# Optimization experiments

Measured on AMD Instinct MI355X. Metric: run time of the kernel, lower is better.

The kernel has to match this reference:

```python
import jax, jax.numpy as jnp
import numpy as np

BITS = 8
KQA_TOPK_PROP = 0.25
NUM_HEADS = 16


def quantize_pc(t, n_bits=BITS):
    # per-channel fake quantization over the last dim (torch quantize with
    # quantization_type='per_channel')
    q_max = 2 ** (n_bits - 1) - 1
    scales = jnp.max(jnp.abs(t), axis=-1, keepdims=True)
    scales = jnp.maximum(scales, 1e-5) / q_max
    return jnp.clip(jnp.round(t / scales), -q_max - 1, q_max) * scales


def setup_inputs() -> dict:
    key = jax.random.key(0)
    ks = jax.random.split(key, 5)
    B, N, C = 4, 1024, 1024
    x = jax.random.normal(ks[0], (B, N, C), dtype=jnp.float32)
    W_qkv = jax.random.normal(ks[1], (3 * C, C), dtype=jnp.float32) * (C ** -0.5)
    b_qkv = jax.random.normal(ks[2], (3 * C,), dtype=jnp.float32) * 0.02
    W_proj = jax.random.normal(ks[3], (C, C), dtype=jnp.float32) * (C ** -0.5)
    b_proj = jax.random.normal(ks[4], (C,), dtype=jnp.float32) * 0.02
    return {"x": x, "W_qkv": W_qkv, "b_qkv": b_qkv, "W_proj": W_proj, "b_proj": b_proj}


def _split_qkv(lin, B, N, H, hd):
    # [B,N,3C] -> (3,B,H,N,hd)
    t = jnp.transpose(lin.reshape(B, N, 3, H, hd), (2, 0, 3, 1, 4))
    return t[0], t[1], t[2]


def reference(x, W_qkv, b_qkv, W_proj, b_proj):
    B, N, C = x.shape
    H = NUM_HEADS
    hd = C // H
    scale = hd ** -0.5

    # --- quantized QKV path (KeyQueryAttention) ---
    q_x = quantize_pc(x)
    q_w = quantize_pc(W_qkv)
    q_b = quantize_pc(b_qkv)
    q_lin = quantize_pc(jnp.einsum('bnc,oc->bno', q_x, q_w) + q_b)
    q_q, q_k, _ = _split_qkv(q_lin, B, N, H, hd)
    q_attn = jnp.einsum('bhnd,bhmd->bhnm', q_q, q_k) * scale

    # --- topk-sliced partial-matmul approximation path ---
    r1 = int(C * KQA_TOPK_PROP) + 1  # channel slice of x / W_qkv
    topk_lin = jnp.einsum('bnc,oc->bno', x[:, :, :r1], W_qkv[:, :r1]) + b_qkv
    topk_q, topk_k, _ = _split_qkv(topk_lin, B, N, H, hd)
    r2 = int(hd * KQA_TOPK_PROP) + 1  # slices the SEQUENCE dim (dim 2), as in the torch code
    topk_attn = jnp.einsum('bhnd,bhmd->bhnm', topk_q[:, :, :r2], topk_k[:, :, :r2]) * scale

    # --- exact attention path (used for the output) ---
    lin = jnp.einsum('bnc,oc->bno', x, W_qkv) + b_qkv
    q, k, v = _split_qkv(lin, B, N, H, hd)
    attn = jax.nn.softmax(jnp.einsum('bhnd,bhmd->bhnm', q, k) * scale, axis=-1)
    out = jnp.einsum('bhnm,bhmd->bhnd', attn, v)  # [B,H,N,hd]
    out = jnp.transpose(out, (0, 2, 1, 3)).reshape(B, N, C)
    out = jnp.einsum('bnc,oc->bno', out, W_proj) + b_proj
    return out, q_attn, topk_attn
```

## Files before the change

### kernel.cpp

```cpp
#include <hip/hip_runtime.h>
#include <stdint.h>

typedef __bf16 bf16x8 __attribute__((ext_vector_type(8)));
typedef float f32x4 __attribute__((ext_vector_type(4)));
typedef int i32x4 __attribute__((ext_vector_type(4)));
typedef unsigned short u16;

#define DEVI static __device__ __forceinline__

DEVI u16 bfu(float f){
  unsigned u = __builtin_bit_cast(unsigned, f);
  unsigned r = u + 0x7fffu + ((u >> 16) & 1u);
  return (u16)(r >> 16);
}
DEVI unsigned packbf(float a, float b){
  return (unsigned)bfu(a) | ((unsigned)bfu(b) << 16);
}

DEVI void gload16(const void* g, void* s){
  __builtin_amdgcn_global_load_lds(
      (const __attribute__((address_space(1))) unsigned int*)g,
      (__attribute__((address_space(3))) unsigned int*)s, 16, 0, 0);
}

DEVI float blockReduceMax(float v, float* sred){
  for (int off = 32; off; off >>= 1) v = fmaxf(v, __shfl_xor(v, off));
  int w = threadIdx.x >> 6;
  if ((threadIdx.x & 63) == 0) sred[w] = v;
  __syncthreads();
  float r = fmaxf(fmaxf(sred[0], sred[1]), fmaxf(sred[2], sred[3]));
  __syncthreads();
  return r;
}

DEVI void quant_row_body(const float* __restrict__ in, int8_t* __restrict__ qo,
                         u16* __restrict__ bo, float* __restrict__ so, int row, float* sred){
  const int t = threadIdx.x;
  const float4 v = *(const float4*)(in + (size_t)row * 1024 + t * 4);
  float am = fmaxf(fmaxf(fabsf(v.x), fabsf(v.y)), fmaxf(fabsf(v.z), fabsf(v.w)));
  am = blockReduceMax(am, sred);
  const float s = fmaxf(am, 1e-5f) / 127.0f;
  if (t == 0) so[row] = s;
  char4 q;
  q.x = (int8_t)(int)fminf(fmaxf(rintf(v.x / s), -128.f), 127.f);
  q.y = (int8_t)(int)fminf(fmaxf(rintf(v.y / s), -128.f), 127.f);
  q.z = (int8_t)(int)fminf(fmaxf(rintf(v.z / s), -128.f), 127.f);
  q.w = (int8_t)(int)fminf(fmaxf(rintf(v.w / s), -128.f), 127.f);
  *(char4*)(qo + (size_t)row * 1024 + t * 4) = q;
  ushort4 h; h.x = bfu(v.x); h.y = bfu(v.y); h.z = bfu(v.z); h.w = bfu(v.w);
  *(ushort4*)(bo + (size_t)row * 1024 + t * 4) = h;
}

DEVI void quant_b_body(const float* __restrict__ b, float* __restrict__ qb, float* sred){
  const int t = threadIdx.x;
  float am = 0.f;
  for (int i = t; i < 3072; i += 256) am = fmaxf(am, fabsf(b[i]));
  am = blockReduceMax(am, sred);
  const float s = fmaxf(am, 1e-5f) / 127.0f;
  for (int i = t; i < 3072; i += 256){
    float q = fminf(fmaxf(rintf(b[i] / s), -128.f), 127.f);
    qb[i] = q * s;
  }
}

DEVI void topk_lin_body(int idx, const float* __restrict__ x, const float* __restrict__ Wq,
                        const float* __restrict__ bq, float* __restrict__ tlin){
  const int o = idx & 2047, bn = idx >> 11;
  const int b_ = bn / 17, n = bn % 17;
  const float* xr = x + ((size_t)b_ * 1024 + n) * 1024;
  const float* wr = Wq + (size_t)o * 1024;
  const float4* x4 = (const float4*)xr;
  const float4* w4 = (const float4*)wr;
  float s = 0.f;
  for (int c = 0; c < 64; c++){
    float4 a = x4[c], b = w4[c];
    s += a.x * b.x + a.y * b.y + a.z * b.z + a.w * b.w;
  }
  s += xr[256] * wr[256];
  tlin[idx] = s + bq[o];
}

DEVI void gemm_i8_body(char* smem, int bid, const int8_t* __restrict__ A, const int8_t* __restrict__ Bm,
    const float* __restrict__ sx, const float* __restrict__ sw, const float* __restrict__ qb,
    float* __restrict__ out){
  int8_t* As = (int8_t*)smem;
  int8_t* Bs = (int8_t*)(smem + 8192);
  const int t = threadIdx.x, l = t & 63, w = t >> 6;
  const int m0 = (bid / 24) * 128, n0 = (bid % 24) * 128;
  const int wm = (w >> 1) * 64, wn = (w & 1) * 64, lr = l & 15, lg = l >> 4;
  i32x4 acc[4][4];
  i32x4 z = {0, 0, 0, 0};
  for (int i = 0; i < 4; i++) for (int j = 0; j < 4; j++) acc[i][j] = z;
  for (int kt = 0; kt < 16; kt++){
    __syncthreads();
    for (int it = 0; it < 2; it++){
      int c = w * 2 + it;
      int idx = c * 64 + l;
      int r = idx >> 2, boff = (idx & 3) * 16;
      gload16(A  + (size_t)(m0 + r) * 1024 + kt * 64 + boff, &As[c * 1024]);
      gload16(Bm + (size_t)(n0 + r) * 1024 + kt * 64 + boff, &Bs[c * 1024]);
    }
    __syncthreads();
    i32x4 a[4], b[4];
    for (int i = 0; i < 4; i++) a[i] = *(const i32x4*)(&As[(wm + i * 16 + lr) * 64 + lg * 16]);
    for (int j = 0; j < 4; j++) b[j] = *(const i32x4*)(&Bs[(wn + j * 16 + lr) * 64 + lg * 16]);
    for (int i = 0; i < 4; i++)
      for (int j = 0; j < 4; j++)
        acc[i][j] = __builtin_amdgcn_mfma_i32_16x16x64_i8(a[i], b[j], acc[i][j], 0, 0, 0);
  }
  for (int i = 0; i < 4; i++){
    int row = m0 + wm + i * 16 + lg * 4;
    for (int j = 0; j < 4; j++){
      int col = n0 + wn + j * 16 + lr;
      float swc = sw[col], qbc = qb[col];
      for (int r = 0; r < 4; r++)
        out[(size_t)(row + r) * 3072 + col] = (float)acc[i][j][r] * sx[row + r] * swc + qbc;
    }
  }
}

template<int MODE>
DEVI void gemm_bf16_body(char* smem, int bid, const u16* __restrict__ A, const u16* __restrict__ Bm,
    const float* __restrict__ bias, void* __restrict__ outp, int K, int N, int nxb){
  u16* As = (u16*)smem;
  u16* Bs = (u16*)(smem + 8192);
  const int t = threadIdx.x, l = t & 63, w = t >> 6;
  const int m0 = (bid / nxb) * 128, n0 = (bid % nxb) * 128;
  const int wm = (w >> 1) * 64, wn = (w & 1) * 64, lr = l & 15, lg = l >> 4;
  f32x4 acc[4][4];
  f32x4 z = {0.f, 0.f, 0.f, 0.f};
  for (int i = 0; i < 4; i++) for (int j = 0; j < 4; j++) acc[i][j] = z;
  const int nkt = K >> 5;
  for (int kt = 0; kt < nkt; kt++){
    __syncthreads();
    for (int it = 0; it < 2; it++){
      int c = w * 2 + it;
      int idx = c * 64 + l;
      int r = idx >> 2, off = (idx & 3) * 8;
      gload16(A  + (size_t)(m0 + r) * K + kt * 32 + off, &As[c * 512]);
      gload16(Bm + (size_t)(n0 + r) * K + kt * 32 + off, &Bs[c * 512]);
    }
    __syncthreads();
    bf16x8 a[4], b[4];
    for (int i = 0; i < 4; i++) a[i] = *(const bf16x8*)(&As[(wm + i * 16 + lr) * 32 + lg * 8]);
    for (int j = 0; j < 4; j++) b[j] = *(const bf16x8*)(&Bs[(wn + j * 16 + lr) * 32 + lg * 8]);
    for (int i = 0; i < 4; i++)
      for (int j = 0; j < 4; j++)
        acc[i][j] = __builtin_amdgcn_mfma_f32_16x16x32_bf16(a[i], b[j], acc[i][j], 0, 0, 0);
  }
  for (int i = 0; i < 4; i++){
    int row = m0 + wm + i * 16 + lg * 4;
    for (int j = 0; j < 4; j++){
      int col = n0 + wn + j * 16 + lr;
      float bc = bias[col];
      for (int r = 0; r < 4; r++){
        float v = acc[i][j][r] + bc;
        if (MODE == 0){
          int s = col >> 10, h = (col >> 6) & 15, d = col & 63;
          int b_ = (row + r) >> 10, n = (row + r) & 1023;
          ((u16*)outp)[(((size_t)(s * 64 + b_ * 16 + h)) * 1024 + n) * 64 + d] = bfu(v);
        } else {
          ((float*)outp)[(size_t)(row + r) * N + col] = v;
        }
      }
    }
  }
}

DEVI void topk_attn_body(int b2, const float* __restrict__ tlin, float* __restrict__ outp){
  const int idx = b2 * 256 + threadIdx.x;
  if (idx >= 4 * 16 * 17 * 17) return;
  const int mm = idx % 17; int rest = idx / 17;
  const int nn = rest % 17; rest /= 17;
  const int h = rest % 16; const int b_ = rest / 16;
  const float* tq = tlin + ((size_t)(b_ * 17 + nn)) * 2048 + h * 64;
  const float* tk = tlin + ((size_t)(b_ * 17 + mm)) * 2048 + 1024 + h * 64;
  float s = 0.f;
  for (int d = 0; d < 64; d++) s += tq[d] * tk[d];
  outp[71303168 + idx] = s * 0.125f;
}

DEVI void qlin_quant_body(float* sred, int row, const float* __restrict__ qlin,
                          float* __restrict__ s_ql, int8_t* __restrict__ iq, int8_t* __restrict__ ik){
  const int t = threadIdx.x;
  const float* rp = qlin + (size_t)row * 3072;
  float am = 0.f;
  for (int i = 0; i < 3; i++){
    float4 v = *(const float4*)(rp + t * 4 + i * 1024);
    am = fmaxf(am, fmaxf(fmaxf(fabsf(v.x), fabsf(v.y)), fmaxf(fabsf(v.z), fabsf(v.w))));
  }
  am = blockReduceMax(am, sred);
  const float s = fmaxf(am, 1e-5f) / 127.0f;
  if (t == 0) s_ql[row] = s;
  const int b_ = row >> 10, n = row & 1023;
  const int o0 = t * 8;
  int8_t* dst = (o0 < 1024) ? iq : ik;
  const int oo = o0 & 1023, h = oo >> 6, d = oo & 63;
  const size_t base = (((size_t)(b_ * 16 + h) * 1024 + n) * 64 + d);
  union { int8_t c[8]; unsigned long long u; } pk;
  for (int j = 0; j < 8; j++)
    pk.c[j] = (int8_t)(int)fminf(fmaxf(rintf(rp[o0 + j] / s), -128.f), 127.f);
  *(unsigned long long*)(dst + base) = pk.u;
}

DEVI void attn_body(u16* vt, int qt, int bz, const u16* __restrict__ qkv, u16* __restrict__ aout){
  const int t = threadIdx.x, l = t & 63, w = t >> 6, lr = l & 15, lg = l >> 4;
  const int b_ = bz >> 4, h = bz & 15;
  const u16* Q  = qkv + (size_t)bz * 65536;
  const u16* Kg = qkv + (size_t)(64 + bz) * 65536;
  const u16* Vg = qkv + (size_t)(128 + bz) * 65536;
  const int q0 = qt * 64 + w * 16;
  const bf16x8 bq0 = *(const bf16x8*)(Q + (size_t)(q0 + lr) * 64 + lg * 8);
  const bf16x8 bq1 = *(const bf16x8*)(Q + (size_t)(q0 + lr) * 64 + 32 + lg * 8);
  float m = -1e30f, lsum = 0.f;
  f32x4 o[4];
  f32x4 zf = {0.f, 0.f, 0.f, 0.f};
  for (int dt = 0; dt < 4; dt++) o[dt] = zf;
  const int hi = lg & 1, tt = lg >> 1;
  const int srcA = lr + 32 * hi, srcB = srcA + 16;
  const int vr = t >> 3, voff = (t & 7) * 8;
  {
    uint4 vv = *(const uint4*)(Vg + (size_t)vr * 64 + voff);
    const u16* pv = (const u16*)&vv;
    for (int j = 0; j < 8; j++) vt[(0 * 64 + voff + j) * 40 + vr] = pv[j];
  }
  __syncthreads();
  int cur = 0;
  for (int kv0 = 0; kv0 < 1024; kv0 += 32){
    const bf16x8 ak00 = *(const bf16x8*)(Kg + (size_t)(kv0 + lr) * 64 + lg * 8);
    const bf16x8 ak01 = *(const bf16x8*)(Kg + (size_t)(kv0 + lr) * 64 + 32 + lg * 8);
    const bf16x8 ak10 = *(const bf16x8*)(Kg + (size_t)(kv0 + 16 + lr) * 64 + lg * 8);
    const bf16x8 ak11 = *(const bf16x8*)(Kg + (size_t)(kv0 + 16 + lr) * 64 + 32 + lg * 8);
    const bool more = (kv0 + 32) < 1024;
    uint4 vn = {0, 0, 0, 0};
    if (more) vn = *(const uint4*)(Vg + (size_t)(kv0 + 32 + vr) * 64 + voff);
    f32x4 st[2];
    {
      f32x4 c = zf;
      c = __builtin_amdgcn_mfma_f32_16x16x32_bf16(ak00, bq0, c, 0, 0, 0);
      c = __builtin_amdgcn_mfma_f32_16x16x32_bf16(ak01, bq1, c, 0, 0, 0);
      st[0] = c;
      c = zf;
      c = __builtin_amdgcn_mfma_f32_16x16x32_bf16(ak10, bq0, c, 0, 0, 0);
      c = __builtin_amdgcn_mfma_f32_16x16x32_bf16(ak11, bq1, c, 0, 0, 0);
      st[1] = c;
    }
    float tmax = -1e30f;
    for (int kvt = 0; kvt < 2; kvt++)
      for (int r = 0; r < 4; r++){ st[kvt][r] *= 0.125f; tmax = fmaxf(tmax, st[kvt][r]); }
    tmax = fmaxf(tmax, __shfl_xor(tmax, 16));
    tmax = fmaxf(tmax, __shfl_xor(tmax, 32));
    const float mn = fmaxf(m, tmax);
    const float f = __expf(m - mn);
    m = mn;
    float p[2][4], psum = 0.f;
    for (int kvt = 0; kvt < 2; kvt++)
      for (int r = 0; r < 4; r++){ float e = __expf(st[kvt][r] - mn); p[kvt][r] = e; psum += e; }
    psum += __shfl_xor(psum, 16);
    psum += __shfl_xor(psum, 32);
    lsum = lsum * f + psum;
    for (int dt = 0; dt < 4; dt++) for (int r = 0; r < 4; r++) o[dt][r] *= f;
    int pk00 = (int)packbf(p[0][0], p[0][1]), pk01 = (int)packbf(p[0][2], p[0][3]);
    int pk10 = (int)packbf(p[1][0], p[1][1]), pk11 = (int)packbf(p[1][2], p[1][3]);
    int a0 = __shfl(pk00, srcA), a1 = __shfl(pk10, srcA);
    int b0 = __shfl(pk01, srcA), b1 = __shfl(pk11, srcA);
    int c0 = __shfl(pk00, srcB), c1 = __shfl(pk10, srcB);
    int d0 = __shfl(pk01, srcB), d1 = __shfl(pk11, srcB);
    union { unsigned u[4]; bf16x8 v; } bp;
    bp.u[0] = (unsigned)(tt ? a1 : a0);
    bp.u[1] = (unsigned)(tt ? b1 : b0);
    bp.u[2] = (unsigned)(tt ? c1 : c0);
    bp.u[3] = (unsigned)(tt ? d1 : d0);
    for (int dt = 0; dt < 4; dt++){
      bf16x8 av = *(const bf16x8*)(&vt[(cur * 64 + dt * 16 + lr) * 40 + lg * 8]);
      o[dt] = __builtin_amdgcn_mfma_f32_16x16x32_bf16(av, bp.v, o[dt], 0, 0, 0);
    }
    if (more){
      const u16* pv = (const u16*)&vn;
      for (int j = 0; j < 8; j++) vt[((cur ^ 1) * 64 + voff + j) * 40 + vr] = pv[j];
    }
    __syncthreads();
    cur ^= 1;
  }
  const float rn = 1.0f / lsum;
  for (int dt = 0; dt < 4; dt++){
    ushort4 hv;
    hv.x = bfu(o[dt][0] * rn); hv.y = bfu(o[dt][1] * rn);
    hv.z = bfu(o[dt][2] * rn); hv.w = bfu(o[dt][3] * rn);
    *(ushort4*)(aout + ((size_t)(b_ * 1024 + q0 + lr)) * 1024 + h * 64 + dt * 16 + lg * 4) = hv;
  }
}

DEVI void qattn_body(int b2, const int8_t* __restrict__ iq, const int8_t* __restrict__ ik,
    const float* __restrict__ s_ql, float* __restrict__ outp){
  const int t = threadIdx.x, l = t & 63, w = t >> 6, lr = l & 15, lg = l >> 4;
  const int n0 = (b2 & 7) * 128, m0 = ((b2 >> 3) & 7) * 128, bz = b2 >> 6;
  const int wm = (w >> 1) * 64, wn = (w & 1) * 64;
  const int b_ = bz >> 4;
  const int8_t* Aq = iq + (size_t)bz * 65536;
  const int8_t* Bk = ik + (size_t)bz * 65536;
  i32x4 a[4], b[4];
  for (int i = 0; i < 4; i++) a[i] = *(const i32x4*)(Aq + (size_t)(m0 + wm + i * 16 + lr) * 64 + lg * 16);
  for (int j = 0; j < 4; j++) b[j] = *(const i32x4*)(Bk + (size_t)(n0 + wn + j * 16 + lr) * 64 + lg * 16);
  float* op = outp + 4194304 + (size_t)bz * 1048576;
  i32x4 z = {0, 0, 0, 0};
  for (int i = 0; i < 4; i++){
    int row = m0 + wm + i * 16 + lg * 4;
    for (int j = 0; j < 4; j++){
      i32x4 acc = __builtin_amdgcn_mfma_i32_16x16x64_i8(a[i], b[j], z, 0, 0, 0);
      int col = n0 + wn + j * 16 + lr;
      float sc = s_ql[b_ * 1024 + col] * 0.125f;
      for (int r = 0; r < 4; r++)
        op[(size_t)(row + r) * 1024 + col] = (float)acc[r] * s_ql[b_ * 1024 + row + r] * sc;
    }
  }
}

__global__ __launch_bounds__(256) void stageA(
    const float* __restrict__ x, const float* __restrict__ Wq, const float* __restrict__ bq,
    const float* __restrict__ Wp,
    int8_t* __restrict__ ix, u16* __restrict__ xb, float* __restrict__ sx,
    int8_t* __restrict__ iw, u16* __restrict__ wb, float* __restrict__ sw,
    float* __restrict__ qbv, u16* __restrict__ Wpb, float* __restrict__ tlin){
  __shared__ float sred[4];
  const int bid = blockIdx.x, t = threadIdx.x;
  if (bid < 4096){
    quant_row_body(x, ix, xb, sx, bid, sred);
  } else if (bid < 7168){
    quant_row_body(Wq, iw, wb, sw, bid - 4096, sred);
  } else if (bid == 7168){
    quant_b_body(bq, qbv, sred);
  } else if (bid < 7169 + 1024){
    const int i = ((bid - 7169) * 256 + t) * 4;
    float4 v = *(const float4*)(Wp + i);
    ushort4 h; h.x = bfu(v.x); h.y = bfu(v.y); h.z = bfu(v.z); h.w = bfu(v.w);
    *(ushort4*)(Wpb + i) = h;
  } else {
    topk_lin_body((bid - 8193) * 256 + t, x, Wq, bq, tlin);
  }
}

__global__ __launch_bounds__(256) void stageB(
    const int8_t* __restrict__ ix, const int8_t* __restrict__ iw, const float* __restrict__ sx,
    const float* __restrict__ sw, const float* __restrict__ qbv, float* __restrict__ qlin,
    const u16* __restrict__ xb, const u16* __restrict__ wb, const float* __restrict__ bq,
    u16* __restrict__ qkv, const float* __restrict__ tlin, float* __restrict__ dout){
  __shared__ __align__(16) char smem[16384];
  const int bid = blockIdx.x;
  if (bid < 768) gemm_i8_body(smem, bid, ix, iw, sx, sw, qbv, qlin);
  else if (bid < 1536) gemm_bf16_body<0>(smem, bid - 768, xb, wb, bq, qkv, 1024, 3072, 24);
  else topk_attn_body(bid - 1536, tlin, dout);
}

__global__ __launch_bounds__(256) void stageC(
    const u16* __restrict__ qkv, u16* __restrict__ aout,
    const float* __restrict__ qlin, float* __restrict__ sql,
    int8_t* __restrict__ iq, int8_t* __restrict__ ik){
  __shared__ __align__(16) char smem[10240];
  const int bid = blockIdx.x;
  if (bid < 1024) attn_body((u16*)smem, bid & 15, bid >> 4, qkv, aout);
  else qlin_quant_body((float*)smem, bid - 1024, qlin, sql, iq, ik);
}

__global__ __launch_bounds__(256) void stageD(
    const u16* __restrict__ aout, const u16* __restrict__ Wpb, const float* __restrict__ bp,
    float* __restrict__ dout,
    const int8_t* __restrict__ iq, const int8_t* __restrict__ ik, const float* __restrict__ sql){
  __shared__ __align__(16) char smem[16384];
  const int bid = blockIdx.x;
  if (bid < 256) gemm_bf16_body<1>(smem, bid, aout, Wpb, bp, dout, 1024, 1024, 8);
  else qattn_body(bid - 256, iq, ik, sql, dout);
}

extern "C" void kernel_launch(void* const* d_in, const int* in_sizes, int n_in,
                              void* d_out, int out_size, void* d_ws, size_t ws_size,
                              hipStream_t stream){
  const float* x  = (const float*)d_in[0];
  const float* Wq = (const float*)d_in[1];
  const float* bq = (const float*)d_in[2];
  const float* Wp = (const float*)d_in[3];
  const float* bp = (const float*)d_in[4];
  char* ws = (char*)d_ws;
  size_t off = 0;
  auto alloc = [&](size_t bytes) -> void* {
    void* p = ws + off; off += (bytes + 255) & ~(size_t)255; return p;
  };
  float*  qlin = (float*) alloc(4096ull * 3072 * 4);
  int8_t* ix   = (int8_t*)alloc(4096ull * 1024);
  int8_t* iw   = (int8_t*)alloc(3072ull * 1024);
  int8_t* iq   = (int8_t*)alloc(64ull * 1024 * 64);
  int8_t* ik   = (int8_t*)alloc(64ull * 1024 * 64);
  u16*    xb   = (u16*)   alloc(4096ull * 1024 * 2);
  u16*    Wb   = (u16*)   alloc(3072ull * 1024 * 2);
  u16*    qkv  = (u16*)   alloc(3ull * 64 * 1024 * 64 * 2);
  u16*    aout = (u16*)   alloc(4096ull * 1024 * 2);
  u16*    Wpb  = (u16*)   alloc(1024ull * 1024 * 2);
  float*  tlin = (float*) alloc(4ull * 17 * 2048 * 4);
  float*  sx   = (float*) alloc(4096 * 4);
  float*  sw   = (float*) alloc(3072 * 4);
  float*  qbv  = (float*) alloc(3072 * 4);
  float*  sql  = (float*) alloc(4096 * 4);
  float*  dout = (float*)d_out;

  stageA<<<8737, 256, 0, stream>>>(x, Wq, bq, Wp, ix, xb, sx, iw, Wb, sw, qbv, Wpb, tlin);
  stageB<<<1609, 256, 0, stream>>>(ix, iw, sx, sw, qbv, qlin, xb, Wb, bq, qkv, tlin, dout);
  stageC<<<5120, 256, 0, stream>>>(qkv, aout, qlin, sql, iq, ik);
  stageD<<<4352, 256, 0, stream>>>(aout, Wpb, bp, dout, iq, ik, sql);
}
```

Before: 278.7 us.

## Deepen GEMM K tiles with swizzled LDS, store qlin as bf16, remap blocks per XCD

Both the int8 and bf16 GEMMs now load K tiles twice as deep (128 int8 / 64 bf16) into doubled shared memory with an XOR-swizzled layout. This halves the number of sync rounds and avoids LDS bank conflicts. The intermediate quantized-linear buffer is stored as bf16 instead of fp32, cutting its write and read traffic. Block indices are remapped so that consecutive tiles land on the same XCD (stride 8) for better L2 locality. Storing qlin in bf16 changes rounding before requantization, which risks accuracy, and the larger LDS footprint may reduce occupancy.

Result: slower. 298.0 us (+6.9%).

```diff
diff --git a/kernel.cpp b/kernel.cpp
--- a/kernel.cpp
+++ b/kernel.cpp
@@ -12,6 +12,10 @@
   unsigned u = __builtin_bit_cast(unsigned, f);
   unsigned r = u + 0x7fffu + ((u >> 16) & 1u);
   return (u16)(r >> 16);
+}
+DEVI float ubf(u16 h){
+  unsigned u = ((unsigned)h) << 16;
+  return __builtin_bit_cast(float, u);
 }
 DEVI unsigned packbf(float a, float b){
   return (unsigned)bfu(a) | ((unsigned)bfu(b) << 16);
@@ -80,33 +84,38 @@
   tlin[idx] = s + bq[o];
 }
 
-DEVI void gemm_i8_body(char* smem, int bid, const int8_t* __restrict__ A, const int8_t* __restrict__ Bm,
+DEVI void gemm_i8_body(char* smem, int tid, const int8_t* __restrict__ A, const int8_t* __restrict__ Bm,
     const float* __restrict__ sx, const float* __restrict__ sw, const float* __restrict__ qb,
-    float* __restrict__ out){
+    u16* __restrict__ out){
   int8_t* As = (int8_t*)smem;
-  int8_t* Bs = (int8_t*)(smem + 8192);
+  int8_t* Bs = (int8_t*)(smem + 16384);
   const int t = threadIdx.x, l = t & 63, w = t >> 6;
-  const int m0 = (bid / 24) * 128, n0 = (bid % 24) * 128;
+  const int m0 = (tid / 24) * 128, n0 = (tid % 24) * 128;
   const int wm = (w >> 1) * 64, wn = (w & 1) * 64, lr = l & 15, lg = l >> 4;
+  const int srow = (l >> 3);
+  const int scol = (((l & 7) ^ srow) << 4);
   i32x4 acc[4][4];
   i32x4 z = {0, 0, 0, 0};
   for (int i = 0; i < 4; i++) for (int j = 0; j < 4; j++) acc[i][j] = z;
-  for (int kt = 0; kt < 16; kt++){
+  const int xr_ = (lr & 7) << 4;
+  for (int kt = 0; kt < 8; kt++){
     __syncthreads();
-    for (int it = 0; it < 2; it++){
-      int c = w * 2 + it;
-      int idx = c * 64 + l;
-      int r = idx >> 2, boff = (idx & 3) * 16;
-      gload16(A  + (size_t)(m0 + r) * 1024 + kt * 64 + boff, &As[c * 1024]);
-      gload16(Bm + (size_t)(n0 + r) * 1024 + kt * 64 + boff, &Bs[c * 1024]);
+    for (int it = 0; it < 4; it++){
+      int c = w * 4 + it;
+      int r = c * 8 + srow;
+      gload16(A  + (size_t)(m0 + r) * 1024 + kt * 128 + scol, &As[c * 1024]);
+      gload16(Bm + (size_t)(n0 + r) * 1024 + kt * 128 + scol, &Bs[c * 1024]);
     }
     __syncthreads();
-    i32x4 a[4], b[4];
-    for (int i = 0; i < 4; i++) a[i] = *(const i32x4*)(&As[(wm + i * 16 + lr) * 64 + lg * 16]);
-    for (int j = 0; j < 4; j++) b[j] = *(const i32x4*)(&Bs[(wn + j * 16 + lr) * 64 + lg * 16]);
-    for (int i = 0; i < 4; i++)
-      for (int j = 0; j < 4; j++)
-        acc[i][j] = __builtin_amdgcn_mfma_i32_16x16x64_i8(a[i], b[j], acc[i][j], 0, 0, 0);
+    for (int kk = 0; kk < 2; kk++){
+      i32x4 a[4], b[4];
+      const int co = (kk * 64 + lg * 16) ^ xr_;
+      for (int i = 0; i < 4; i++) a[i] = *(const i32x4*)(&As[(wm + i * 16 + lr) * 128 + co]);
+      for (int j = 0; j < 4; j++) b[j] = *(const i32x4*)(&Bs[(wn + j * 16 + lr) * 128 + co]);
+      for (int i = 0; i < 4; i++)
+        for (int j = 0; j < 4; j++)
+          acc[i][j] = __builtin_amdgcn_mfma_i32_16x16x64_i8(a[i], b[j], acc[i][j], 0, 0, 0);
+    }
   }
   for (int i = 0; i < 4; i++){
     int row = m0 + wm + i * 16 + lg * 4;
@@ -114,39 +123,44 @@
       int col = n0 + wn + j * 16 + lr;
       float swc = sw[col], qbc = qb[col];
       for (int r = 0; r < 4; r++)
-        out[(size_t)(row + r) * 3072 + col] = (float)acc[i][j][r] * sx[row + r] * swc + qbc;
+        out[(size_t)(row + r) * 3072 + col] = bfu((float)acc[i][j][r] * sx[row + r] * swc + qbc);
     }
   }
 }
 
 template<int MODE>
-DEVI void gemm_bf16_body(char* smem, int bid, const u16* __restrict__ A, const u16* __restrict__ Bm,
+DEVI void gemm_bf16_body(char* smem, int tid, const u16* __restrict__ A, const u16* __restrict__ Bm,
     const float* __restrict__ bias, void* __restrict__ outp, int K, int N, int nxb){
   u16* As = (u16*)smem;
-  u16* Bs = (u16*)(smem + 8192);
+  u16* Bs = (u16*)(smem + 16384);
   const int t = threadIdx.x, l = t & 63, w = t >> 6;
-  const int m0 = (bid / nxb) * 128, n0 = (bid % nxb) * 128;
+  const int m0 = (tid / nxb) * 128, n0 = (tid % nxb) * 128;
   const int wm = (w >> 1) * 64, wn = (w & 1) * 64, lr = l & 15, lg = l >> 4;
+  const int srow = (l >> 3);
+  const int scol = (((l & 7) ^ srow) << 3);
   f32x4 acc[4][4];
   f32x4 z = {0.f, 0.f, 0.f, 0.f};
   for (int i = 0; i < 4; i++) for (int j = 0; j < 4; j++) acc[i][j] = z;
-  const int nkt = K >> 5;
+  const int nkt = K >> 6;
+  const int xr_ = (lr & 7) << 3;
   for (int kt = 0; kt < nkt; kt++){
     __syncthreads();
-    for (int it = 0; it < 2; it++){
-      int c = w * 2 + it;
-      int idx = c * 64 + l;
-      int r = idx >> 2, off = (idx & 3) * 8;
-      gload16(A  + (size_t)(m0 + r) * K + kt * 32 + off, &As[c * 512]);
-      gload16(Bm + (size_t)(n0 + r) * K + kt * 32 + off, &Bs[c * 512]);
+    for (int it = 0; it < 4; it++){
+      int c = w * 4 + it;
+      int r = c * 8 + srow;
+      gload16(A  + (size_t)(m0 + r) * K + kt * 64 + scol, &As[c * 512]);
+      gload16(Bm + (size_t)(n0 + r) * K + kt * 64 + scol, &Bs[c * 512]);
     }
     __syncthreads();
-    bf16x8 a[4], b[4];
-    for (int i = 0; i < 4; i++) a[i] = *(const bf16x8*)(&As[(wm + i * 16 + lr) * 32 + lg * 8]);
-    for (int j = 0; j < 4; j++) b[j] = *(const bf16x8*)(&Bs[(wn + j * 16 + lr) * 32 + lg * 8]);
-    for (int i = 0; i < 4; i++)
-      for (int j = 0; j < 4; j++)
-        acc[i][j] = __builtin_amdgcn_mfma_f32_16x16x32_bf16(a[i], b[j], acc[i][j], 0, 0, 0);
+    for (int kk = 0; kk < 2; kk++){
+      bf16x8 a[4], b[4];
+      const int co = (kk * 32 + lg * 8) ^ xr_;
+      for (int i = 0; i < 4; i++) a[i] = *(const bf16x8*)(&As[(wm + i * 16 + lr) * 64 + co]);
+      for (int j = 0; j < 4; j++) b[j] = *(const bf16x8*)(&Bs[(wn + j * 16 + lr) * 64 + co]);
+      for (int i = 0; i < 4; i++)
+        for (int j = 0; j < 4; j++)
+          acc[i][j] = __builtin_amdgcn_mfma_f32_16x16x32_bf16(a[i], b[j], acc[i][j], 0, 0, 0);
+    }
   }
   for (int i = 0; i < 4; i++){
     int row = m0 + wm + i * 16 + lg * 4;
@@ -180,14 +194,15 @@
   outp[71303168 + idx] = s * 0.125f;
 }
 
-DEVI void qlin_quant_body(float* sred, int row, const float* __restrict__ qlin,
+DEVI void qlin_quant_body(float* sred, int row, const u16* __restrict__ qlin,
                           float* __restrict__ s_ql, int8_t* __restrict__ iq, int8_t* __restrict__ ik){
   const int t = threadIdx.x;
-  const float* rp = qlin + (size_t)row * 3072;
+  const u16* rp = qlin + (size_t)row * 3072;
   float am = 0.f;
   for (int i = 0; i < 3; i++){
-    float4 v = *(const float4*)(rp + t * 4 + i * 1024);
-    am = fmaxf(am, fmaxf(fmaxf(fabsf(v.x), fabsf(v.y)), fmaxf(fabsf(v.z), fabsf(v.w))));
+    ushort4 v = *(const ushort4*)(rp + t * 4 + i * 1024);
+    am = fmaxf(am, fmaxf(fmaxf(fabsf(ubf(v.x)), fabsf(ubf(v.y))),
+                         fmaxf(fabsf(ubf(v.z)), fabsf(ubf(v.w)))));
   }
   am = blockReduceMax(am, sred);
   const float s = fmaxf(am, 1e-5f) / 127.0f;
@@ -197,9 +212,17 @@
   int8_t* dst = (o0 < 1024) ? iq : ik;
   const int oo = o0 & 1023, h = oo >> 6, d = oo & 63;
   const size_t base = (((size_t)(b_ * 16 + h) * 1024 + n) * 64 + d);
+  ushort4 v0 = *(const ushort4*)(rp + o0);
+  ushort4 v1 = *(const ushort4*)(rp + o0 + 4);
   union { int8_t c[8]; unsigned long long u; } pk;
-  for (int j = 0; j < 8; j++)
-    pk.c[j] = (int8_t)(int)fminf(fmaxf(rintf(rp[o0 + j] / s), -128.f), 127.f);
+  pk.c[0] = (int8_t)(int)fminf(fmaxf(rintf(ubf(v0.x) / s), -128.f), 127.f);
+  pk.c[1] = (int8_t)(int)fminf(fmaxf(rintf(ubf(v0.y) / s), -128.f), 127.f);
+  pk.c[2] = (int8_t)(int)fminf(fmaxf(rintf(ubf(v0.z) / s), -128.f), 127.f);
+  pk.c[3] = (int8_t)(int)fminf(fmaxf(rintf(ubf(v0.w) / s), -128.f), 127.f);
+  pk.c[4] = (int8_t)(int)fminf(fmaxf(rintf(ubf(v1.x) / s), -128.f), 127.f);
+  pk.c[5] = (int8_t)(int)fminf(fmaxf(rintf(ubf(v1.y) / s), -128.f), 127.f);
+  pk.c[6] = (int8_t)(int)fminf(fmaxf(rintf(ubf(v1.z) / s), -128.f), 127.f);
+  pk.c[7] = (int8_t)(int)fminf(fmaxf(rintf(ubf(v1.w) / s), -128.f), 127.f);
   *(unsigned long long*)(dst + base) = pk.u;
 }
 
@@ -342,23 +365,31 @@
 
 __global__ __launch_bounds__(256) void stageB(
     const int8_t* __restrict__ ix, const int8_t* __restrict__ iw, const float* __restrict__ sx,
-    const float* __restrict__ sw, const float* __restrict__ qbv, float* __restrict__ qlin,
+    const float* __restrict__ sw, const float* __restrict__ qbv, u16* __restrict__ qlin,
     const u16* __restrict__ xb, const u16* __restrict__ wb, const float* __restrict__ bq,
     u16* __restrict__ qkv, const float* __restrict__ tlin, float* __restrict__ dout){
-  __shared__ __align__(16) char smem[16384];
+  __shared__ __align__(16) char smem[32768];
   const int bid = blockIdx.x;
-  if (bid < 768) gemm_i8_body(smem, bid, ix, iw, sx, sw, qbv, qlin);
-  else if (bid < 1536) gemm_bf16_body<0>(smem, bid - 768, xb, wb, bq, qkv, 1024, 3072, 24);
-  else topk_attn_body(bid - 1536, tlin, dout);
+  if (bid < 768){
+    const int tid = (bid & 7) * 96 + (bid >> 3);
+    gemm_i8_body(smem, tid, ix, iw, sx, sw, qbv, qlin);
+  } else if (bid < 1536){
+    const int g = bid - 768;
+    const int tid = (g & 7) * 96 + (g >> 3);
+    gemm_bf16_body<0>(smem, tid, xb, wb, bq, qkv, 1024, 3072, 24);
+  } else topk_attn_body(bid - 1536, tlin, dout);
 }
 
 __global__ __launch_bounds__(256) void stageC(
     const u16* __restrict__ qkv, u16* __restrict__ aout,
-    const float* __restrict__ qlin, float* __restrict__ sql,
+    const u16* __restrict__ qlin, float* __restrict__ sql,
     int8_t* __restrict__ iq, int8_t* __restrict__ ik){
   __shared__ __align__(16) char smem[10240];
   const int bid = blockIdx.x;
-  if (bid < 1024) attn_body((u16*)smem, bid & 15, bid >> 4, qkv, aout);
+  if (bid < 1024){
+    const int wk = (bid & 7) * 128 + (bid >> 3);
+    attn_body((u16*)smem, wk & 15, wk >> 4, qkv, aout);
+  }
   else qlin_quant_body((float*)smem, bid - 1024, qlin, sql, iq, ik);
 }
 
@@ -366,10 +397,14 @@
     const u16* __restrict__ aout, const u16* __restrict__ Wpb, const float* __restrict__ bp,
     float* __restrict__ dout,
     const int8_t* __restrict__ iq, const int8_t* __restrict__ ik, const float* __restrict__ sql){
-  __shared__ __align__(16) char smem[16384];
+  __shared__ __align__(16) char smem[32768];
   const int bid = blockIdx.x;
   if (bid < 256) gemm_bf16_body<1>(smem, bid, aout, Wpb, bp, dout, 1024, 1024, 8);
-  else qattn_body(bid - 256, iq, ik, sql, dout);
+  else {
+    const int g = bid - 256;
+    const int w = (g & 7) * 512 + (g >> 3);
+    qattn_body(w, iq, ik, sql, dout);
+  }
 }
 
 extern "C" void kernel_launch(void* const* d_in, const int* in_sizes, int n_in,
@@ -385,7 +420,7 @@
   auto alloc = [&](size_t bytes) -> void* {
     void* p = ws + off; off += (bytes + 255) & ~(size_t)255; return p;
   };
-  float*  qlin = (float*) alloc(4096ull * 3072 * 4);
+  u16*    qlin = (u16*)   alloc(4096ull * 3072 * 2);
   int8_t* ix   = (int8_t*)alloc(4096ull * 1024);
   int8_t* iw   = (int8_t*)alloc(3072ull * 1024);
   int8_t* iq   = (int8_t*)alloc(64ull * 1024 * 64);
```
